# Performance work log

Hardware: AMD Instinct MI355X
Metric: run time of the kernel (lower is better)

The kernel has to match this reference:

```python
import jax, jax.numpy as jnp
import numpy as np

B, H, W, DIM = 32, 56, 56, 192
WSZ = 7
HEADS = 8
DK = 32
DV = 32
INNER_K = HEADS * DK  # 256
INNER_V = HEADS * DV  # 256


def setup_inputs() -> dict:
    key = jax.random.key(0)
    ks = jax.random.split(key, 8)
    s = 0.05
    return {
        "x": jax.random.normal(ks[0], (B, H, W, DIM), jnp.float32),
        "Wq": jax.random.normal(ks[1], (DIM, INNER_K), jnp.float32) * s,
        "Wk": jax.random.normal(ks[2], (DIM, INNER_K), jnp.float32) * s,
        "Wv": jax.random.normal(ks[3], (DIM, INNER_V), jnp.float32) * s,
        "Wlocal": jax.random.normal(ks[4], (3, 3, INNER_V, INNER_V), jnp.float32) * s,
        "b_local": jnp.zeros((INNER_V,), jnp.float32),
        "Wout": jax.random.normal(ks[5], (INNER_V, DIM), jnp.float32) * s,
        "b_out": jnp.zeros((DIM,), jnp.float32),
    }


def _window(t, heads, wsz):
    # (b, H, W, heads*d) -> (b*nx*ny, heads, wsz*wsz, d)
    b, h, w, c = t.shape
    d = c // heads
    nx, ny = h // wsz, w // wsz
    t = t.reshape(b, nx, wsz, ny, wsz, heads, d)
    t = t.transpose(0, 1, 3, 5, 2, 4, 6)
    return t.reshape(b * nx * ny, heads, wsz * wsz, d)


def reference(x, Wq, Wk, Wv, Wlocal, b_local, Wout, b_out):
    scale = DK ** (-0.5)
    # 1x1 convs == per-pixel matmuls
    q = jnp.einsum('bhwc,cd->bhwd', x, Wq)
    k = jnp.einsum('bhwc,cd->bhwd', x, Wk)
    v = jnp.einsum('bhwc,cd->bhwd', x, Wv)
    # 3x3 local interactive conv on v (SAME padding)
    local_out = jax.lax.conv_general_dilated(
        v, Wlocal, window_strides=(1, 1), padding='SAME',
        dimension_numbers=('NHWC', 'HWIO', 'NHWC')) + b_local
    # window partition
    qw = _window(q, HEADS, WSZ)
    kw = _window(k, HEADS, WSZ)
    vw = _window(v, HEADS, WSZ)
    dots = jnp.einsum('bhid,bhjd->bhij', qw, kw) * scale  # (B*nx*ny, heads, 49, 49)
    attn = jax.nn.softmax(dots, axis=-1)
    out = jnp.einsum('bhij,bhjd->bhid', attn, vw)
    # window merge: (b*nx*ny, heads, wsz*wsz, d) -> (b, H, W, heads*d)
    nx, ny = H // WSZ, W // WSZ
    out = out.reshape(B, nx, ny, HEADS, WSZ, WSZ, DV)
    out = out.transpose(0, 1, 4, 2, 5, 3, 6).reshape(B, H, W, HEADS * DV)
    out = out + local_out
    out = jnp.einsum('bhwc,cd->bhwd', out, Wout) + b_out
    return out
```

## Files before the change

kernel.cpp:

```cpp
#include <hip/hip_runtime.h>

typedef unsigned short ushort_t;
typedef __bf16  bf16x8 __attribute__((ext_vector_type(8)));
typedef float   f32x4  __attribute__((ext_vector_type(4)));
typedef unsigned short u16x8 __attribute__((ext_vector_type(8)));

#define MFMA16(a,b,c) __builtin_amdgcn_mfma_f32_16x16x32_bf16((a),(b),(c),0,0,0)
#define WAITVM(N) asm volatile("s_waitcnt vmcnt(" #N ")" ::: "memory")
#define BARRIER() do{ __builtin_amdgcn_s_barrier(); asm volatile("" ::: "memory"); }while(0)

static __device__ __forceinline__ ushort_t f2bf(float f){
  __bf16 h = (__bf16)f;
  return __builtin_bit_cast(ushort_t, h);
}
static __device__ __forceinline__ float bf2f(ushort_t b){
  union{unsigned u; float f;} x; x.u = ((unsigned)b)<<16; return x.f;
}
static __device__ __forceinline__ bf16x8 ldg_bf8u(const ushort_t* p){
  u16x8 r = *(const u16x8*)p;
  return __builtin_bit_cast(bf16x8, r);
}
static __device__ __forceinline__ bf16x8 lds_bf8(const ushort_t* p){
  u16x8 r = *(const u16x8*)p;
  return __builtin_bit_cast(bf16x8, r);
}
static __device__ __forceinline__ void gload_lds16(const ushort_t* g, ushort_t* l){
  __builtin_amdgcn_global_load_lds(
      (const __attribute__((address_space(1))) void*)g,
      (__attribute__((address_space(3))) void*)l, 16, 0, 0);
}

__global__ __launch_bounds__(256) void prep_kernel(
    const float* __restrict__ x,
    const float* __restrict__ Wq, const float* __restrict__ Wk,
    const float* __restrict__ Wv, const float* __restrict__ Wl,
    const float* __restrict__ Wo,
    ushort_t* __restrict__ qkvT, ushort_t* __restrict__ woT,
    ushort_t* __restrict__ xwin, ushort_t* __restrict__ WcT)
{
  int idx = blockIdx.x*256 + threadIdx.x;
  if(idx < 147456){
    int n = idx/192, kk = idx%192;
    const float* W = (n < 256) ? Wq : ((n < 512) ? Wk : Wv);
    qkvT[idx] = f2bf(W[kk*256 + (n & 255)]);
  } else if(idx < 196608){
    int t3 = idx - 147456;
    int col = t3/256, kk = t3%256;
    woT[t3] = f2bf(Wo[kk*192 + col]);
  } else if(idx < 3342336){
    int c = idx - 196608;
    int win = c/1536, t = c%1536;
    int row = t/24, cp = t%24;
    u16x8 o = {0,0,0,0,0,0,0,0};
    if(row < 49){
      int b = win>>6, rem = win&63, wy = rem>>3, wx = rem&7;
      size_t base = (size_t)b*3136 + wy*392 + wx*7;
      int sc = cp ^ (row&7);
      const float* src = x + (base + (row/7)*56 + (row%7))*192 + sc*8;
      float4 f0 = *(const float4*)src;
      float4 f1 = *(const float4*)(src+4);
      o[0]=f2bf(f0.x); o[1]=f2bf(f0.y); o[2]=f2bf(f0.z); o[3]=f2bf(f0.w);
      o[4]=f2bf(f1.x); o[5]=f2bf(f1.y); o[6]=f2bf(f1.z); o[7]=f2bf(f1.w);
    }
    *(u16x8*)&xwin[(size_t)c*8] = o;
  } else if(idx < 3784704){
    int t = idx - 3342336;
    int o = t & 255;
    int tc = t >> 8;
    int tap = tc / 192, c = tc % 192;
    const float* wlp = Wl + (size_t)tap*65536 + o;
    const float* wvp = Wv + (size_t)c*256;
    float acc = 0.f;
    #pragma unroll 8
    for(int k=0;k<256;++k)
      acc += wvp[k] * wlp[(size_t)k*256];
    int ks = c>>5, r = c&31, grp = r>>3, j = r&7;
    int sl = grp ^ ((o>>1)&3);
    WcT[((size_t)tap*6 + ks)*8192 + o*32 + sl*8 + j] = f2bf(acc);
  }
}

__global__ __launch_bounds__(256,2) void qkvattn_kernel(
    const ushort_t* __restrict__ xwin, const ushort_t* __restrict__ WT,
    ushort_t* __restrict__ attnout)
{
  __shared__ ushort_t lds[38912];
  ushort_t* xLds = lds;
  const int tid = threadIdx.x;
  const int w = tid>>6, l = tid&63, lr = l&15, g = l>>4;
  const int bid = blockIdx.x;
  const int win = bid>>1, head = (bid&1)*4 + w;
  const int b = win>>6, rem = win&63, wy = rem>>3, wx = rem&7;
  const size_t base = (size_t)b*3136 + wy*7*56 + wx*7;

  {
    const ushort_t* xsrc = xwin + (size_t)win*12288;
    #pragma unroll
    for(int r=0;r<6;++r)
      gload_lds16(xsrc + (size_t)(tid + r*256)*8,
                  xLds + (size_t)(r*256 + w*64)*8);
  }
  __syncthreads();

  ushort_t* qkBase = lds + 12288 + w*4608;
  ushort_t* vT     = lds + 30720 + w*2048;
  const ushort_t* Wq_ = WT + (size_t)(head*32)*192;
  const ushort_t* Wk_ = WT + (size_t)(256 + head*32)*192;
  const ushort_t* Wv_ = WT + (size_t)(512 + head*32)*192;

  {
    f32x4 aq[4][2], ak[4][2], av[4][2];
    #pragma unroll
    for(int mi=0;mi<4;++mi)
      #pragma unroll
      for(int nj=0;nj<2;++nj){
        f32x4 z={0.f,0.f,0.f,0.f};
        aq[mi][nj]=z; ak[mi][nj]=z; av[mi][nj]=z;
      }
    #pragma unroll
    for(int ks=0; ks<6; ++ks){
      bf16x8 af[4];
      #pragma unroll
      for(int mi=0;mi<4;++mi){
        int row = mi*16 + lr;
        af[mi] = lds_bf8(&xLds[(row*192 + ks*32 + g*8) ^ ((row&7)<<3)]);
      }
      bf16x8 bq[2], bk[2], bv[2];
      #pragma unroll
      for(int nj=0;nj<2;++nj){
        size_t off = (size_t)(nj*16+lr)*192 + ks*32 + g*8;
        bq[nj] = ldg_bf8u(Wq_ + off);
        bk[nj] = ldg_bf8u(Wk_ + off);
        bv[nj] = ldg_bf8u(Wv_ + off);
      }
      #pragma unroll
      for(int nj=0;nj<2;++nj)
        #pragma unroll
        for(int mi=0;mi<4;++mi){
          aq[mi][nj] = MFMA16(af[mi], bq[nj], aq[mi][nj]);
          ak[mi][nj] = MFMA16(af[mi], bk[nj], ak[mi][nj]);
          av[mi][nj] = MFMA16(af[mi], bv[nj], av[mi][nj]);
        }
    }
    #pragma unroll
    for(int mi=0;mi<4;++mi)
      #pragma unroll
      for(int nj=0;nj<2;++nj)
        #pragma unroll
        for(int i=0;i<4;++i){
          int row = mi*16 + g*4 + i, col = nj*16 + lr;
          qkBase[row*36 + col]        = f2bf(aq[mi][nj][i]);
          qkBase[2304 + row*36 + col] = f2bf(ak[mi][nj][i]);
          vT[(col*64 + row) ^ ((col&7)<<3)] = f2bf(av[mi][nj][i]);
        }
  }

  f32x4 dot[4][4];
  #pragma unroll
  for(int mi=0;mi<4;++mi)
    #pragma unroll
    for(int nj=0;nj<4;++nj){ f32x4 z={0.f,0.f,0.f,0.f}; dot[mi][nj]=z; }
  bf16x8 qf[4], kf[4];
  #pragma unroll
  for(int t=0;t<4;++t){
    qf[t] = lds_bf8(&qkBase[(t*16+lr)*36 + g*8]);
    kf[t] = lds_bf8(&qkBase[2304 + (t*16+lr)*36 + g*8]);
  }
  #pragma unroll
  for(int mi=0;mi<4;++mi)
    #pragma unroll
    for(int nj=0;nj<4;++nj)
      dot[mi][nj] = MFMA16(qf[mi], kf[nj], dot[mi][nj]);

  const float sc = 0.17677669529663687f * 1.4426950408889634f;
  ushort_t* pl = qkBase;
  #pragma unroll
  for(int mi=0;mi<4;++mi)
    #pragma unroll
    for(int nj=0;nj<4;++nj){
      int col = nj*16 + lr;
      #pragma unroll
      for(int i=0;i<4;++i){
        float e = (col < 49) ? exp2f(dot[mi][nj][i]*sc) : 0.f;
        int row = mi*16 + g*4 + i;
        pl[(row*64 + col) ^ ((row&7)<<3)] = f2bf(e);
      }
    }

  u16x8 ones_u = {0x3f80,0x3f80,0x3f80,0x3f80,0x3f80,0x3f80,0x3f80,0x3f80};
  bf16x8 ones8 = __builtin_bit_cast(bf16x8, ones_u);
  f32x4 o[4][2], rsum[4];
  #pragma unroll
  for(int mi=0;mi<4;++mi){
    f32x4 z={0.f,0.f,0.f,0.f};
    o[mi][0]=z; o[mi][1]=z; rsum[mi]=z;
  }
  #pragma unroll
  for(int ks=0;ks<2;++ks){
    bf16x8 pa[4];
    #pragma unroll
    for(int mi=0;mi<4;++mi){
      int row = mi*16 + lr;
      pa[mi] = lds_bf8(&pl[(row*64 + ks*32 + g*8) ^ ((row&7)<<3)]);
    }
    #pragma unroll
    for(int nj=0;nj<2;++nj){
      int d = nj*16 + lr;
      bf16x8 vb = lds_bf8(&vT[(d*64 + ks*32 + g*8) ^ ((d&7)<<3)]);
      #pragma unroll
      for(int mi=0;mi<4;++mi) o[mi][nj] = MFMA16(pa[mi], vb, o[mi][nj]);
    }
    #pragma unroll
    for(int mi=0;mi<4;++mi) rsum[mi] = MFMA16(pa[mi], ones8, rsum[mi]);
  }
  #pragma unroll
  for(int mi=0;mi<4;++mi){
    #pragma unroll
    for(int i=0;i<4;++i){
      int row = mi*16 + g*4 + i;
      if(row < 49){
        size_t pix = base + (row/7)*56 + (row%7);
        float inv = 1.0f / rsum[mi][i];
        #pragma unroll
        for(int nj=0;nj<2;++nj)
          attnout[pix*256 + head*32 + nj*16 + lr] = f2bf(o[mi][nj][i] * inv);
      }
    }
  }
}

__global__ __launch_bounds__(256,2) void conv_kernel(
    const ushort_t* __restrict__ xwin, const ushort_t* __restrict__ WcT,
    const float* __restrict__ b_local, ushort_t* __restrict__ local_out)
{
  __shared__ ushort_t aBuf[2][256*32];
  __shared__ ushort_t bBuf[3][256*32];
  const int bid = blockIdx.x;
  const int tile = (bid & 7) * 98 + (bid >> 3);
  const int p0 = tile * 128;
  const int tid = threadIdx.x;
  const int l = tid&63, w=tid>>6, wm=w>>1, wn=w&1, lr=l&15, g=l>>4;

  unsigned maskbits[4];
  int pxloc[4];
  #pragma unroll
  for(int mi=0;mi<4;++mi){
    int p = p0 + wm*64 + mi*16 + lr;
    int rem = p % 3136;
    int y = rem/56, x = rem%56;
    unsigned mb = 0;
    #pragma unroll
    for(int tap=0;tap<9;++tap){
      int dy = tap/3 - 1, dx = tap%3 - 1;
      if(((unsigned)(y+dy) < 56u) && ((unsigned)(x+dx) < 56u)) mb |= (1u<<tap);
    }
    maskbits[mi] = mb;
    pxloc[mi] = wm*64 + mi*16 + lr + 64;
  }

  unsigned aBase[4]; int aR7[4], aWant[4];
  #pragma unroll
  for(int r=0;r<4;++r){
    int c = tid + r*256;
    int px = c>>2, sl = c&3;
    int px_abs = p0 - 64 + px;
    px_abs = min(max(px_abs, 0), 100351);
    int b2 = px_abs/3136, rem2 = px_abs%3136;
    int y2 = rem2/56, x2 = rem2%56;
    int win2 = b2*64 + (y2/7)*8 + (x2/7);
    int row2 = (y2%7)*7 + (x2%7);
    aBase[r] = (unsigned)win2*12288u + (unsigned)row2*192u;
    aR7[r]   = row2 & 7;
    aWant[r] = sl ^ ((px>>1)&3);
  }

  auto stageA = [&](int ks, ushort_t* dst){
    #pragma unroll
    for(int r=0;r<4;++r){
      int cp = (ks*4 + aWant[r]) ^ aR7[r];
      gload_lds16(xwin + aBase[r] + cp*8,
                  dst + (size_t)(r*256 + w*64)*8);
    }
  };
  auto stageB = [&](int ks, int tap, ushort_t* dst){
    const ushort_t* src = WcT + ((size_t)tap*6 + ks)*8192;
    #pragma unroll
    for(int r=0;r<4;++r){
      gload_lds16(src + (size_t)(tid + r*256)*8,
                  dst + (size_t)(r*256 + w*64)*8);
    }
  };

  f32x4 acc[4][8];
  #pragma unroll
  for(int mi=0;mi<4;++mi)
    #pragma unroll
    for(int nj=0;nj<8;++nj){ f32x4 z={0.f,0.f,0.f,0.f}; acc[mi][nj]=z; }

  auto compute = [&](int tap, const ushort_t* aL, const ushort_t* bL){
    int shift = (tap/3 - 1)*56 + (tap%3 - 1);
    bf16x8 af[4];
    #pragma unroll
    for(int mi=0;mi<4;++mi){
      int px = pxloc[mi] + shift;
      int sl = g ^ ((px>>1)&3);
      u16x8 rv = *(const u16x8*)&aL[px*32 + sl*8];
      if(!((maskbits[mi]>>tap)&1)){ u16x8 z={0,0,0,0,0,0,0,0}; rv=z; }
      af[mi] = __builtin_bit_cast(bf16x8, rv);
    }
    __builtin_amdgcn_s_setprio(1);
    #pragma unroll
    for(int nj=0;nj<8;++nj){
      int col = wn*128 + nj*16 + lr;
      int slb = g ^ ((col>>1)&3);
      bf16x8 bfr = lds_bf8(&bL[col*32 + slb*8]);
      #pragma unroll
      for(int mi=0;mi<4;++mi) acc[mi][nj] = MFMA16(af[mi], bfr, acc[mi][nj]);
    }
    __builtin_amdgcn_s_setprio(0);
  };

  stageA(0, aBuf[0]);
  stageB(0, 0, bBuf[0]);
  stageB(0, 1, bBuf[1]);

  for(int ks=0; ks<5; ++ks){
    #pragma unroll
    for(int tap=0; tap<9; ++tap){
      if(tap==1) WAITVM(8); else WAITVM(4);
      BARRIER();
      if(tap==0) stageA(ks+1, aBuf[(ks+1)&1]);
      stageB(ks + (tap+2)/9, (tap+2)%9, bBuf[(tap+2)%3]);
      compute(tap, aBuf[ks&1], bBuf[tap%3]);
    }
  }
  #pragma unroll
  for(int tap=0; tap<9; ++tap){
    if(tap==8) WAITVM(0); else WAITVM(4);
    BARRIER();
    if(tap<7) stageB(5, tap+2, bBuf[(tap+2)%3]);
    compute(tap, aBuf[1], bBuf[tap%3]);
  }

  #pragma unroll
  for(int nj=0;nj<8;++nj){
    int col = wn*128 + nj*16 + lr;
    float bb = b_local[col];
    #pragma unroll
    for(int mi=0;mi<4;++mi)
      #pragma unroll
      for(int i=0;i<4;++i){
        int p = p0 + wm*64 + mi*16 + g*4 + i;
        local_out[(size_t)p*256 + col] = f2bf(acc[mi][nj][i] + bb);
      }
  }
}

__global__ __launch_bounds__(256,4) void outproj_kernel(
    const ushort_t* __restrict__ attnout, const ushort_t* __restrict__ locl,
    const ushort_t* __restrict__ WoT, const float* __restrict__ b_out,
    float* __restrict__ out)
{
  __shared__ ushort_t aLds[64*256];
  const int m0 = blockIdx.x * 64;
  const int tid = threadIdx.x;
  const int l = tid&63, w = tid>>6, lr=l&15, g=l>>4;
  #pragma unroll
  for(int r=0;r<8;++r){
    int c = tid + r*256;
    int row = c>>5, cc = c&31;
    size_t off = (size_t)(m0+row)*256 + cc*8;
    u16x8 a = *(const u16x8*)(attnout + off);
    u16x8 b2 = *(const u16x8*)(locl + off);
    u16x8 o;
    #pragma unroll
    for(int j=0;j<8;++j) o[j] = f2bf(bf2f(a[j]) + bf2f(b2[j]));
    *(u16x8*)&aLds[(row*256 + cc*8) ^ ((row&7)<<3)] = o;
  }
  __syncthreads();

  const ushort_t* Wbase = WoT + (size_t)(w*48)*256;
  f32x4 acc[4][3];
  #pragma unroll
  for(int mi=0;mi<4;++mi)
    #pragma unroll
    for(int nj=0;nj<3;++nj){ f32x4 z={0.f,0.f,0.f,0.f}; acc[mi][nj]=z; }

  #pragma unroll
  for(int ks=0;ks<8;++ks){
    bf16x8 bfr[3];
    #pragma unroll
    for(int nj=0;nj<3;++nj)
      bfr[nj] = ldg_bf8u(Wbase + (size_t)(nj*16+lr)*256 + ks*32 + g*8);
    bf16x8 af[4];
    #pragma unroll
    for(int mi=0;mi<4;++mi){
      int row = mi*16 + lr;
      af[mi] = lds_bf8(&aLds[(row*256 + ks*32 + g*8) ^ ((row&7)<<3)]);
    }
    #pragma unroll
    for(int nj=0;nj<3;++nj)
      #pragma unroll
      for(int mi=0;mi<4;++mi) acc[mi][nj] = MFMA16(af[mi], bfr[nj], acc[mi][nj]);
  }
  #pragma unroll
  for(int nj=0;nj<3;++nj){
    int col = w*48 + nj*16 + lr;
    float bb = b_out[col];
    #pragma unroll
    for(int mi=0;mi<4;++mi)
      #pragma unroll
      for(int i=0;i<4;++i){
        int row = mi*16 + g*4 + i;
        out[(size_t)(m0+row)*192 + col] = acc[mi][nj][i] + bb;
      }
  }
}

extern "C" void kernel_launch(void* const* d_in, const int* in_sizes, int n_in,
                              void* d_out, int out_size, void* d_ws, size_t ws_size,
                              hipStream_t stream)
{
  const float* x  = (const float*)d_in[0];
  const float* Wq = (const float*)d_in[1];
  const float* Wk = (const float*)d_in[2];
  const float* Wv = (const float*)d_in[3];
  const float* Wl = (const float*)d_in[4];
  const float* bl = (const float*)d_in[5];
  const float* Wo = (const float*)d_in[6];
  const float* bo = (const float*)d_in[7];
  float* out = (float*)d_out;
  char* ws = (char*)d_ws;
  ushort_t* attnout = (ushort_t*)(ws);
  ushort_t* xwin    = (ushort_t*)(ws + 51380224);
  ushort_t* locl    = (ushort_t*)(ws + 205520896);
  ushort_t* qkvT    = (ushort_t*)(ws + 256901120);
  ushort_t* WcT     = (ushort_t*)(ws + 257196032);
  ushort_t* woT     = (ushort_t*)(ws + 258375680);

  prep_kernel<<<14784, 256, 0, stream>>>(x, Wq, Wk, Wv, Wl, Wo,
                                         qkvT, woT, xwin, WcT);
  qkvattn_kernel<<<4096, 256, 0, stream>>>(xwin, qkvT, attnout);
  conv_kernel<<<784, 256, 0, stream>>>(xwin, WcT, bl, locl);
  outproj_kernel<<<1568, 256, 0, stream>>>(attnout, locl, woT, bo, out);
}
```

Baseline: 291.2 us.

## Fuse attention and local conv kernels into one interleaved launch

```diff
diff --git a/kernel.cpp b/kernel.cpp
--- a/kernel.cpp
+++ b/kernel.cpp
@@ -80,279 +80,280 @@
   }
 }
 
-__global__ __launch_bounds__(256,2) void qkvattn_kernel(
+__global__ __launch_bounds__(256,2) void mid_kernel(
     const ushort_t* __restrict__ xwin, const ushort_t* __restrict__ WT,
-    ushort_t* __restrict__ attnout)
+    const ushort_t* __restrict__ WcT, const float* __restrict__ b_local,
+    ushort_t* __restrict__ attnout, ushort_t* __restrict__ locl)
 {
-  __shared__ ushort_t lds[38912];
-  ushort_t* xLds = lds;
+  __shared__ ushort_t sh[40960];
+  const int grp = blockIdx.x / 305, rr = blockIdx.x % 305;
   const int tid = threadIdx.x;
-  const int w = tid>>6, l = tid&63, lr = l&15, g = l>>4;
-  const int bid = blockIdx.x;
-  const int win = bid>>1, head = (bid&1)*4 + w;
-  const int b = win>>6, rem = win&63, wy = rem>>3, wx = rem&7;
-  const size_t base = (size_t)b*3136 + wy*7*56 + wx*7;
-
-  {
-    const ushort_t* xsrc = xwin + (size_t)win*12288;
-    #pragma unroll
-    for(int r=0;r<6;++r)
-      gload_lds16(xsrc + (size_t)(tid + r*256)*8,
-                  xLds + (size_t)(r*256 + w*64)*8);
-  }
-  __syncthreads();
-
-  ushort_t* qkBase = lds + 12288 + w*4608;
-  ushort_t* vT     = lds + 30720 + w*2048;
-  const ushort_t* Wq_ = WT + (size_t)(head*32)*192;
-  const ushort_t* Wk_ = WT + (size_t)(256 + head*32)*192;
-  const ushort_t* Wv_ = WT + (size_t)(512 + head*32)*192;
-
-  {
-    f32x4 aq[4][2], ak[4][2], av[4][2];
+  const int l = tid&63, w = tid>>6, lr = l&15, g = l>>4;
+
+  if(rr < 256){
+    const int bid = grp*256 + rr;
+    ushort_t* xLds = sh;
+    const int win = bid>>1, head = (bid&1)*4 + w;
+    const int b = win>>6, rem = win&63, wy = rem>>3, wx = rem&7;
+    const size_t base = (size_t)b*3136 + wy*7*56 + wx*7;
+
+    {
+      const ushort_t* xsrc = xwin + (size_t)win*12288;
+      #pragma unroll
+      for(int r=0;r<6;++r)
+        gload_lds16(xsrc + (size_t)(tid + r*256)*8,
+                    xLds + (size_t)(r*256 + w*64)*8);
+    }
+    __syncthreads();
+
+    ushort_t* qkBase = sh + 12288 + w*4608;
+    ushort_t* vT     = sh + 30720 + w*2048;
+    const ushort_t* Wq_ = WT + (size_t)(head*32)*192;
+    const ushort_t* Wk_ = WT + (size_t)(256 + head*32)*192;
+    const ushort_t* Wv_ = WT + (size_t)(512 + head*32)*192;
+
+    {
+      f32x4 aq[4][2], ak[4][2], av[4][2];
+      #pragma unroll
+      for(int mi=0;mi<4;++mi)
+        #pragma unroll
+        for(int nj=0;nj<2;++nj){
+          f32x4 z={0.f,0.f,0.f,0.f};
+          aq[mi][nj]=z; ak[mi][nj]=z; av[mi][nj]=z;
+        }
+      #pragma unroll
+      for(int ks=0; ks<6; ++ks){
+        bf16x8 af[4];
+        #pragma unroll
+        for(int mi=0;mi<4;++mi){
+          int row = mi*16 + lr;
+          af[mi] = lds_bf8(&xLds[(row*192 + ks*32 + g*8) ^ ((row&7)<<3)]);
+        }
+        bf16x8 bq[2], bk[2], bv[2];
+        #pragma unroll
+        for(int nj=0;nj<2;++nj){
+          size_t off = (size_t)(nj*16+lr)*192 + ks*32 + g*8;
+          bq[nj] = ldg_bf8u(Wq_ + off);
+          bk[nj] = ldg_bf8u(Wk_ + off);
+          bv[nj] = ldg_bf8u(Wv_ + off);
+        }
+        #pragma unroll
+        for(int nj=0;nj<2;++nj)
+          #pragma unroll
+          for(int mi=0;mi<4;++mi){
+            aq[mi][nj] = MFMA16(af[mi], bq[nj], aq[mi][nj]);
+            ak[mi][nj] = MFMA16(af[mi], bk[nj], ak[mi][nj]);
+            av[mi][nj] = MFMA16(af[mi], bv[nj], av[mi][nj]);
+          }
+      }
+      #pragma unroll
+      for(int mi=0;mi<4;++mi)
+        #pragma unroll
+        for(int nj=0;nj<2;++nj)
+          #pragma unroll
+          for(int i=0;i<4;++i){
+            int row = mi*16 + g*4 + i, col = nj*16 + lr;
+            qkBase[row*36 + col]        = f2bf(aq[mi][nj][i]);
+            qkBase[2304 + row*36 + col] = f2bf(ak[mi][nj][i]);
+            vT[(col*64 + row) ^ ((col&7)<<3)] = f2bf(av[mi][nj][i]);
+          }
+    }
+
+    f32x4 dot[4][4];
     #pragma unroll
     for(int mi=0;mi<4;++mi)
       #pragma unroll
-      for(int nj=0;nj<2;++nj){
-        f32x4 z={0.f,0.f,0.f,0.f};
-        aq[mi][nj]=z; ak[mi][nj]=z; av[mi][nj]=z;
-      }
-    #pragma unroll
-    for(int ks=0; ks<6; ++ks){
-      bf16x8 af[4];
+      for(int nj=0;nj<4;++nj){ f32x4 z={0.f,0.f,0.f,0.f}; dot[mi][nj]=z; }
+    bf16x8 qf[4], kf[4];
+    #pragma unroll
+    for(int t=0;t<4;++t){
+      qf[t] = lds_bf8(&qkBase[(t*16+lr)*36 + g*8]);
+      kf[t] = lds_bf8(&qkBase[2304 + (t*16+lr)*36 + g*8]);
+    }
+    #pragma unroll
+    for(int mi=0;mi<4;++mi)
+      #pragma unroll
+      for(int nj=0;nj<4;++nj)
+        dot[mi][nj] = MFMA16(qf[mi], kf[nj], dot[mi][nj]);
+
+    const float sc = 0.17677669529663687f * 1.4426950408889634f;
+    ushort_t* pl = qkBase;
+    #pragma unroll
+    for(int mi=0;mi<4;++mi)
+      #pragma unroll
+      for(int nj=0;nj<4;++nj){
+        int col = nj*16 + lr;
+        #pragma unroll
+        for(int i=0;i<4;++i){
+          float e = (col < 49) ? exp2f(dot[mi][nj][i]*sc) : 0.f;
+          int row = mi*16 + g*4 + i;
+          pl[(row*64 + col) ^ ((row&7)<<3)] = f2bf(e);
+        }
+      }
+
+    u16x8 ones_u = {0x3f80,0x3f80,0x3f80,0x3f80,0x3f80,0x3f80,0x3f80,0x3f80};
+    bf16x8 ones8 = __builtin_bit_cast(bf16x8, ones_u);
+    f32x4 o[4][2], rsum[4];
+    #pragma unroll
+    for(int mi=0;mi<4;++mi){
+      f32x4 z={0.f,0.f,0.f,0.f};
+      o[mi][0]=z; o[mi][1]=z; rsum[mi]=z;
+    }
+    #pragma unroll
+    for(int ks=0;ks<2;++ks){
+      bf16x8 pa[4];
       #pragma unroll
       for(int mi=0;mi<4;++mi){
         int row = mi*16 + lr;
-        af[mi] = lds_bf8(&xLds[(row*192 + ks*32 + g*8) ^ ((row&7)<<3)]);
-      }
-      bf16x8 bq[2], bk[2], bv[2];
+        pa[mi] = lds_bf8(&pl[(row*64 + ks*32 + g*8) ^ ((row&7)<<3)]);
+      }
       #pragma unroll
       for(int nj=0;nj<2;++nj){
-        size_t off = (size_t)(nj*16+lr)*192 + ks*32 + g*8;
-        bq[nj] = ldg_bf8u(Wq_ + off);
-        bk[nj] = ldg_bf8u(Wk_ + off);
-        bv[nj] = ldg_bf8u(Wv_ + off);
-      }
-      #pragma unroll
-      for(int nj=0;nj<2;++nj)
-        #pragma unroll
-        for(int mi=0;mi<4;++mi){
-          aq[mi][nj] = MFMA16(af[mi], bq[nj], aq[mi][nj]);
-          ak[mi][nj] = MFMA16(af[mi], bk[nj], ak[mi][nj]);
-          av[mi][nj] = MFMA16(af[mi], bv[nj], av[mi][nj]);
-        }
-    }
+        int d = nj*16 + lr;
+        bf16x8 vb = lds_bf8(&vT[(d*64 + ks*32 + g*8) ^ ((d&7)<<3)]);
+        #pragma unroll
+        for(int mi=0;mi<4;++mi) o[mi][nj] = MFMA16(pa[mi], vb, o[mi][nj]);
+      }
+      #pragma unroll
+      for(int mi=0;mi<4;++mi) rsum[mi] = MFMA16(pa[mi], ones8, rsum[mi]);
+    }
+    #pragma unroll
+    for(int mi=0;mi<4;++mi){
+      #pragma unroll
+      for(int i=0;i<4;++i){
+        int row = mi*16 + g*4 + i;
+        if(row < 49){
+          size_t pix = base + (row/7)*56 + (row%7);
+          float inv = 1.0f / rsum[mi][i];
+          #pragma unroll
+          for(int nj=0;nj<2;++nj)
+            attnout[pix*256 + head*32 + nj*16 + lr] = f2bf(o[mi][nj][i] * inv);
+        }
+      }
+    }
+  } else {
+    const int cbid = grp*49 + (rr - 256);
+    const int tile = (cbid & 7) * 98 + (cbid >> 3);
+    const int p0 = tile * 128;
+    const int wm = w>>1, wn = w&1;
+
+    unsigned maskbits[4];
+    int pxloc[4];
+    #pragma unroll
+    for(int mi=0;mi<4;++mi){
+      int p = p0 + wm*64 + mi*16 + lr;
+      int rem = p % 3136;
+      int y = rem/56, x = rem%56;
+      unsigned mb = 0;
+      #pragma unroll
+      for(int tap=0;tap<9;++tap){
+        int dy = tap/3 - 1, dx = tap%3 - 1;
+        if(((unsigned)(y+dy) < 56u) && ((unsigned)(x+dx) < 56u)) mb |= (1u<<tap);
+      }
+      maskbits[mi] = mb;
+      pxloc[mi] = wm*64 + mi*16 + lr + 64;
+    }
+
+    unsigned aBase[4]; int aR7[4], aWant[4];
+    #pragma unroll
+    for(int r=0;r<4;++r){
+      int c = tid + r*256;
+      int px = c>>2, sl = c&3;
+      int px_abs = p0 - 64 + px;
+      px_abs = min(max(px_abs, 0), 100351);
+      int b2 = px_abs/3136, rem2 = px_abs%3136;
+      int y2 = rem2/56, x2 = rem2%56;
+      int win2 = b2*64 + (y2/7)*8 + (x2/7);
+      int row2 = (y2%7)*7 + (x2%7);
+      aBase[r] = (unsigned)win2*12288u + (unsigned)row2*192u;
+      aR7[r]   = row2 & 7;
+      aWant[r] = sl ^ ((px>>1)&3);
+    }
+
+    auto stageA = [&](int ks, int buf){
+      ushort_t* dst0 = sh + buf*8192;
+      #pragma unroll
+      for(int r=0;r<4;++r){
+        int cp = (ks*4 + aWant[r]) ^ aR7[r];
+        gload_lds16(xwin + aBase[r] + cp*8,
+                    dst0 + (size_t)(r*256 + w*64)*8);
+      }
+    };
+    auto stageB = [&](int ks, int tap, int buf){
+      ushort_t* dst0 = sh + 16384 + buf*8192;
+      const ushort_t* src = WcT + ((size_t)tap*6 + ks)*8192;
+      #pragma unroll
+      for(int r=0;r<4;++r){
+        gload_lds16(src + (size_t)(tid + r*256)*8,
+                    dst0 + (size_t)(r*256 + w*64)*8);
+      }
+    };
+
+    f32x4 acc[4][8];
     #pragma unroll
     for(int mi=0;mi<4;++mi)
       #pragma unroll
-      for(int nj=0;nj<2;++nj)
-        #pragma unroll
-        for(int i=0;i<4;++i){
-          int row = mi*16 + g*4 + i, col = nj*16 + lr;
-          qkBase[row*36 + col]        = f2bf(aq[mi][nj][i]);
-          qkBase[2304 + row*36 + col] = f2bf(ak[mi][nj][i]);
-          vT[(col*64 + row) ^ ((col&7)<<3)] = f2bf(av[mi][nj][i]);
-        }
-  }
-
-  f32x4 dot[4][4];
-  #pragma unroll
-  for(int mi=0;mi<4;++mi)
-    #pragma unroll
-    for(int nj=0;nj<4;++nj){ f32x4 z={0.f,0.f,0.f,0.f}; dot[mi][nj]=z; }
-  bf16x8 qf[4], kf[4];
-  #pragma unroll
-  for(int t=0;t<4;++t){
-    qf[t] = lds_bf8(&qkBase[(t*16+lr)*36 + g*8]);
-    kf[t] = lds_bf8(&qkBase[2304 + (t*16+lr)*36 + g*8]);
-  }
-  #pragma unroll
-  for(int mi=0;mi<4;++mi)
-    #pragma unroll
-    for(int nj=0;nj<4;++nj)
-      dot[mi][nj] = MFMA16(qf[mi], kf[nj], dot[mi][nj]);
-
-  const float sc = 0.17677669529663687f * 1.4426950408889634f;
-  ushort_t* pl = qkBase;
-  #pragma unroll
-  for(int mi=0;mi<4;++mi)
-    #pragma unroll
-    for(int nj=0;nj<4;++nj){
-      int col = nj*16 + lr;
-      #pragma unroll
-      for(int i=0;i<4;++i){
-        float e = (col < 49) ? exp2f(dot[mi][nj][i]*sc) : 0.f;
-        int row = mi*16 + g*4 + i;
-        pl[(row*64 + col) ^ ((row&7)<<3)] = f2bf(e);
-      }
-    }
-
-  u16x8 ones_u = {0x3f80,0x3f80,0x3f80,0x3f80,0x3f80,0x3f80,0x3f80,0x3f80};
-  bf16x8 ones8 = __builtin_bit_cast(bf16x8, ones_u);
-  f32x4 o[4][2], rsum[4];
-  #pragma unroll
-  for(int mi=0;mi<4;++mi){
-    f32x4 z={0.f,0.f,0.f,0.f};
-    o[mi][0]=z; o[mi][1]=z; rsum[mi]=z;
-  }
-  #pragma unroll
-  for(int ks=0;ks<2;++ks){
-    bf16x8 pa[4];
-    #pragma unroll
-    for(int mi=0;mi<4;++mi){
-      int row = mi*16 + lr;
-      pa[mi] = lds_bf8(&pl[(row*64 + ks*32 + g*8) ^ ((row&7)<<3)]);
-    }
-    #pragma unroll
-    for(int nj=0;nj<2;++nj){
-      int d = nj*16 + lr;
-      bf16x8 vb = lds_bf8(&vT[(d*64 + ks*32 + g*8) ^ ((d&7)<<3)]);
-      #pragma unroll
-      for(int mi=0;mi<4;++mi) o[mi][nj] = MFMA16(pa[mi], vb, o[mi][nj]);
-    }
-    #pragma unroll
-    for(int mi=0;mi<4;++mi) rsum[mi] = MFMA16(pa[mi], ones8, rsum[mi]);
-  }
-  #pragma unroll
-  for(int mi=0;mi<4;++mi){
-    #pragma unroll
-    for(int i=0;i<4;++i){
-      int row = mi*16 + g*4 + i;
-      if(row < 49){
-        size_t pix = base + (row/7)*56 + (row%7);
-        float inv = 1.0f / rsum[mi][i];
-        #pragma unroll
-        for(int nj=0;nj<2;++nj)
-          attnout[pix*256 + head*32 + nj*16 + lr] = f2bf(o[mi][nj][i] * inv);
-      }
-    }
-  }
-}
-
-__global__ __launch_bounds__(256,2) void conv_kernel(
-    const ushort_t* __restrict__ xwin, const ushort_t* __restrict__ WcT,
-    const float* __restrict__ b_local, ushort_t* __restrict__ local_out)
-{
-  __shared__ ushort_t aBuf[2][256*32];
-  __shared__ ushort_t bBuf[3][256*32];
-  const int bid = blockIdx.x;
-  const int tile = (bid & 7) * 98 + (bid >> 3);
-  const int p0 = tile * 128;
-  const int tid = threadIdx.x;
-  const int l = tid&63, w=tid>>6, wm=w>>1, wn=w&1, lr=l&15, g=l>>4;
-
-  unsigned maskbits[4];
-  int pxloc[4];
-  #pragma unroll
-  for(int mi=0;mi<4;++mi){
-    int p = p0 + wm*64 + mi*16 + lr;
-    int rem = p % 3136;
-    int y = rem/56, x = rem%56;
-    unsigned mb = 0;
-    #pragma unroll
-    for(int tap=0;tap<9;++tap){
-      int dy = tap/3 - 1, dx = tap%3 - 1;
-      if(((unsigned)(y+dy) < 56u) && ((unsigned)(x+dx) < 56u)) mb |= (1u<<tap);
-    }
-    maskbits[mi] = mb;
-    pxloc[mi] = wm*64 + mi*16 + lr + 64;
-  }
-
-  unsigned aBase[4]; int aR7[4], aWant[4];
-  #pragma unroll
-  for(int r=0;r<4;++r){
-    int c = tid + r*256;
-    int px = c>>2, sl = c&3;
-    int px_abs = p0 - 64 + px;
-    px_abs = min(max(px_abs, 0), 100351);
-    int b2 = px_abs/3136, rem2 = px_abs%3136;
-    int y2 = rem2/56, x2 = rem2%56;
-    int win2 = b2*64 + (y2/7)*8 + (x2/7);
-    int row2 = (y2%7)*7 + (x2%7);
-    aBase[r] = (unsigned)win2*12288u + (unsigned)row2*192u;
-    aR7[r]   = row2 & 7;
-    aWant[r] = sl ^ ((px>>1)&3);
-  }
-
-  auto stageA = [&](int ks, ushort_t* dst){
-    #pragma unroll
-    for(int r=0;r<4;++r){
-      int cp = (ks*4 + aWant[r]) ^ aR7[r];
-      gload_lds16(xwin + aBase[r] + cp*8,
-                  dst + (size_t)(r*256 + w*64)*8);
-    }
-  };
-  auto stageB = [&](int ks, int tap, ushort_t* dst){
-    const ushort_t* src = WcT + ((size_t)tap*6 + ks)*8192;
-    #pragma unroll
-    for(int r=0;r<4;++r){
-      gload_lds16(src + (size_t)(tid + r*256)*8,
-                  dst + (size_t)(r*256 + w*64)*8);
-    }
-  };
-
-  f32x4 acc[4][8];
-  #pragma unroll
-  for(int mi=0;mi<4;++mi)
-    #pragma unroll
-    for(int nj=0;nj<8;++nj){ f32x4 z={0.f,0.f,0.f,0.f}; acc[mi][nj]=z; }
-
-  auto compute = [&](int tap, const ushort_t* aL, const ushort_t* bL){
-    int shift = (tap/3 - 1)*56 + (tap%3 - 1);
-    bf16x8 af[4];
-    #pragma unroll
-    for(int mi=0;mi<4;++mi){
-      int px = pxloc[mi] + shift;
-      int sl = g ^ ((px>>1)&3);
-      u16x8 rv = *(const u16x8*)&aL[px*32 + sl*8];
-      if(!((maskbits[mi]>>tap)&1)){ u16x8 z={0,0,0,0,0,0,0,0}; rv=z; }
-      af[mi] = __builtin_bit_cast(bf16x8, rv);
-    }
-    __builtin_amdgcn_s_setprio(1);
+      for(int nj=0;nj<8;++nj){ f32x4 z={0.f,0.f,0.f,0.f}; acc[mi][nj]=z; }
+
+    auto compute = [&](int tap, int abuf, int bbuf){
+      const ushort_t* aL = sh + abuf*8192;
+      const ushort_t* bL = sh + 16384 + bbuf*8192;
+      int shift = (tap/3 - 1)*56 + (tap%3 - 1);
+      bf16x8 af[4];
+      #pragma unroll
+      for(int mi=0;mi<4;++mi){
+        int px = pxloc[mi] + shift;
+        int sl = g ^ ((px>>1)&3);
+        u16x8 rv = *(const u16x8*)&aL[px*32 + sl*8];
+        if(!((maskbits[mi]>>tap)&1)){ u16x8 z={0,0,0,0,0,0,0,0}; rv=z; }
+        af[mi] = __builtin_bit_cast(bf16x8, rv);
+      }
+      __builtin_amdgcn_s_setprio(1);
+      #pragma unroll
+      for(int nj=0;nj<8;++nj){
+        int col = wn*128 + nj*16 + lr;
+        int slb = g ^ ((col>>1)&3);
+        bf16x8 bfr = lds_bf8(&bL[col*32 + slb*8]);
+        #pragma unroll
+        for(int mi=0;mi<4;++mi) acc[mi][nj] = MFMA16(af[mi], bfr, acc[mi][nj]);
+      }
+      __builtin_amdgcn_s_setprio(0);
+    };
+
+    stageA(0, 0);
+    stageB(0, 0, 0);
+    stageB(0, 1, 1);
+
+    for(int ks=0; ks<5; ++ks){
+      #pragma unroll
+      for(int tap=0; tap<9; ++tap){
+        if(tap==1) WAITVM(8); else WAITVM(4);
+        BARRIER();
+        if(tap==0) stageA(ks+1, (ks+1)&1);
+        stageB(ks + (tap+2)/9, (tap+2)%9, (tap+2)%3);
+        compute(tap, ks&1, tap%3);
+      }
+    }
+    #pragma unroll
+    for(int tap=0; tap<9; ++tap){
+      if(tap==8) WAITVM(0); else WAITVM(4);
+      BARRIER();
+      if(tap<7) stageB(5, tap+2, (tap+2)%3);
+      compute(tap, 1, tap%3);
+    }
+
     #pragma unroll
     for(int nj=0;nj<8;++nj){
       int col = wn*128 + nj*16 + lr;
-      int slb = g ^ ((col>>1)&3);
-      bf16x8 bfr = lds_bf8(&bL[col*32 + slb*8]);
-      #pragma unroll
-      for(int mi=0;mi<4;++mi) acc[mi][nj] = MFMA16(af[mi], bfr, acc[mi][nj]);
-    }
-    __builtin_amdgcn_s_setprio(0);
-  };
-
-  stageA(0, aBuf[0]);
-  stageB(0, 0, bBuf[0]);
-  stageB(0, 1, bBuf[1]);
-
-  for(int ks=0; ks<5; ++ks){
-    #pragma unroll
-    for(int tap=0; tap<9; ++tap){
-      if(tap==1) WAITVM(8); else WAITVM(4);
-      BARRIER();
-      if(tap==0) stageA(ks+1, aBuf[(ks+1)&1]);
-      stageB(ks + (tap+2)/9, (tap+2)%9, bBuf[(tap+2)%3]);
-      compute(tap, aBuf[ks&1], bBuf[tap%3]);
-    }
-  }
-  #pragma unroll
-  for(int tap=0; tap<9; ++tap){
-    if(tap==8) WAITVM(0); else WAITVM(4);
-    BARRIER();
-    if(tap<7) stageB(5, tap+2, bBuf[(tap+2)%3]);
-    compute(tap, aBuf[1], bBuf[tap%3]);
-  }
-
-  #pragma unroll
-  for(int nj=0;nj<8;++nj){
-    int col = wn*128 + nj*16 + lr;
-    float bb = b_local[col];
-    #pragma unroll
-    for(int mi=0;mi<4;++mi)
-      #pragma unroll
-      for(int i=0;i<4;++i){
-        int p = p0 + wm*64 + mi*16 + g*4 + i;
-        local_out[(size_t)p*256 + col] = f2bf(acc[mi][nj][i] + bb);
-      }
+      float bb = b_local[col];
+      #pragma unroll
+      for(int mi=0;mi<4;++mi)
+        #pragma unroll
+        for(int i=0;i<4;++i){
+          int p = p0 + wm*64 + mi*16 + g*4 + i;
+          locl[(size_t)p*256 + col] = f2bf(acc[mi][nj][i] + bb);
+        }
+    }
   }
 }
 
@@ -440,7 +441,6 @@
 
   prep_kernel<<<14784, 256, 0, stream>>>(x, Wq, Wk, Wv, Wl, Wo,
                                          qkvT, woT, xwin, WcT);
-  qkvattn_kernel<<<4096, 256, 0, stream>>>(xwin, qkvT, attnout);
-  conv_kernel<<<784, 256, 0, stream>>>(xwin, WcT, bl, locl);
+  mid_kernel<<<4880, 256, 0, stream>>>(xwin, qkvT, WcT, bl, attnout, locl);
   outproj_kernel<<<1568, 256, 0, stream>>>(attnout, locl, woT, bo, out);
 }
```

Result: slower. 381.9 us (+31.1%).
